# Performance work log

Hardware: AMD Instinct MI355X
Metric: run time of the kernel (lower is better)

Reference implementation:

```python
import jax, jax.numpy as jnp
import numpy as np

B, S, D = 2, 2048, 1024
H_Q, H_KV, DK, DV = 16, 8, 64, 64
R = H_Q // H_KV  # q heads per kv head (GQA)
THETA = 10000.0


def setup_inputs() -> dict:
    key = jax.random.key(0)
    ks = jax.random.split(key, 12)
    inv_freq = 1.0 / (THETA ** (jnp.arange(0, DK, 2, dtype=jnp.float32) / DK))  # [DK/2]
    angles = jnp.arange(S, dtype=jnp.float32)[:, None] * inv_freq[None, :]      # [S, DK/2]
    scale = 0.02
    return {
        "x": jax.random.normal(ks[0], (B, S, D), jnp.float32),
        "Wq": jax.random.normal(ks[1], (D, H_Q * DK), jnp.float32) * scale,
        "bq": jnp.zeros((H_Q * DK,), jnp.float32),
        "Wk": jax.random.normal(ks[2], (D, H_KV * DK), jnp.float32) * scale,
        "bk": jnp.zeros((H_KV * DK,), jnp.float32),
        "Wv": jax.random.normal(ks[3], (D, H_KV * DV), jnp.float32) * scale,
        "bv": jnp.zeros((H_KV * DV,), jnp.float32),
        "Wo": jax.random.normal(ks[4], (H_Q * DV, D), jnp.float32) * scale,
        "bo": jnp.zeros((D,), jnp.float32),
        "freqs_cos": jnp.cos(angles),
        "freqs_sin": jnp.sin(angles),
        "attention_mask": jax.random.bernoulli(ks[5], 0.9, (B, S)),  # True = real token
    }


def _rope(t, cos, sin):
    # t: [B, S, H, Dh]; cos/sin: [S, Dh/2]. Complex rotation on interleaved pairs.
    tp = t.reshape(*t.shape[:-1], -1, 2)
    x1, x2 = tp[..., 0], tp[..., 1]
    c = cos[None, :, None, :]
    s = sin[None, :, None, :]
    o1 = x1 * c - x2 * s
    o2 = x1 * s + x2 * c
    return jnp.stack([o1, o2], axis=-1).reshape(t.shape)


def reference(x, Wq, bq, Wk, bk, Wv, bv, Wo, bo, freqs_cos, freqs_sin, attention_mask):
    b, s, _ = x.shape
    q = (x @ Wq + bq).reshape(b, s, H_Q, DK)
    k = (x @ Wk + bk).reshape(b, s, H_KV, DK)
    v = (x @ Wv + bv).reshape(b, s, H_KV, DV)
    q = _rope(q, freqs_cos, freqs_sin)
    k = _rope(k, freqs_cos, freqs_sin)
    q = q.transpose(0, 2, 1, 3)                      # [B, Hq, S, DK]
    k = jnp.repeat(k.transpose(0, 2, 1, 3), R, axis=1)  # GQA expand -> [B, Hq, S, DK]
    v = jnp.repeat(v.transpose(0, 2, 1, 3), R, axis=1)  # [B, Hq, S, DV]
    causal = jnp.tril(jnp.ones((s, s), dtype=bool))
    # Module does logical_or(padding, causal) -- replicated faithfully.
    mask = jnp.logical_or(attention_mask[:, None, None, :], causal[None, None])
    scale = 1.0 / jnp.sqrt(jnp.float32(DK))
    scores = jnp.einsum('bhqd,bhkd->bhqk', q, k) * scale
    scores = jnp.where(mask, scores, -jnp.inf)
    attn = jax.nn.softmax(scores, axis=-1)
    out = jnp.einsum('bhqk,bhkd->bhqd', attn, v)
    out = out.transpose(0, 2, 1, 3).reshape(b, s, H_Q * DV)
    return out @ Wo + bo
```

## Files before the change

### kernel.cpp

```cpp
#include <hip/hip_runtime.h>
#include <hip/hip_bf16.h>
#include <math.h>

typedef __attribute__((ext_vector_type(8))) short bf16x8;
typedef __attribute__((ext_vector_type(4))) float f32x4;

#define OFF_XB  0ull
#define OFF_WT  (8ull<<20)
#define OFF_WO  (12ull<<20)
#define OFF_QB  (14ull<<20)
#define OFF_KB  (22ull<<20)
#define OFF_VT  (26ull<<20)
#define OFF_AO  (30ull<<20)
#define OFF_MB  (38ull<<20)

#define QSCALE 0.18033688056680276f

__device__ inline unsigned pack_bf162(float a, float b) {
    __hip_bfloat162 t = __float22bfloat162_rn(make_float2(a, b));
    return *(unsigned*)&t;
}

__device__ inline float exp2_fast(float x) {
    float r;
    asm("v_exp_f32 %0, %1" : "=v"(r) : "v"(x));
    return r;
}

__device__ inline void gload16(const void* g, void* l) {
    __builtin_amdgcn_global_load_lds(
        (const __attribute__((address_space(1))) void*)g,
        (__attribute__((address_space(3))) void*)l, 16, 0, 0);
}

__launch_bounds__(256)
__global__ void prep_kernel(const float* __restrict__ x,
                            const float* __restrict__ Wq, const float* __restrict__ Wk,
                            const float* __restrict__ Wv, const float* __restrict__ Wo,
                            const void* __restrict__ mraw,
                            __hip_bfloat16* __restrict__ XB,
                            __hip_bfloat16* __restrict__ WT,
                            __hip_bfloat16* __restrict__ WoT,
                            float* __restrict__ mbias) {
    __shared__ float T[32][33];
    __shared__ int bad01, badf;
    const int tid = threadIdx.x;
    const int bid = blockIdx.x;
    if (bid < 1024) {
        const int base = bid * 4096;
#pragma unroll
        for (int i = 0; i < 4; ++i) {
            const int e = base + (i * 256 + tid) * 4;
            const float4 v = *(const float4*)&x[e];
            uint2 pk;
            pk.x = pack_bf162(v.x, v.y);
            pk.y = pack_bf162(v.z, v.w);
            *(uint2*)&XB[e] = pk;
        }
    } else if (bid < 4096) {
        const float* src; int ldn, nbase; __hip_bfloat16* dst; int n0, k0;
        if (bid < 3072) {
            const int tb = bid - 1024;
            const int kt = tb >> 6, nt = tb & 63;
            n0 = nt * 32; k0 = kt * 32; dst = WT;
            if (n0 < 1024)      { src = Wq; ldn = 1024; nbase = n0; }
            else if (n0 < 1536) { src = Wk; ldn = 512;  nbase = n0 - 1024; }
            else                { src = Wv; ldn = 512;  nbase = n0 - 1536; }
        } else {
            const int tb = bid - 3072;
            const int kt = tb >> 5, nt = tb & 31;
            n0 = nt * 32; k0 = kt * 32; dst = WoT;
            src = Wo; ldn = 1024; nbase = n0;
        }
        const int c = tid & 31, r0 = tid >> 5;
#pragma unroll
        for (int i = 0; i < 4; ++i)
            T[r0 + 8 * i][c] = src[(size_t)(k0 + r0 + 8 * i) * ldn + nbase + c];
        __syncthreads();
#pragma unroll
        for (int i = 0; i < 4; ++i) {
            const int nn = r0 + 8 * i;
            dst[(size_t)(n0 + nn) * 1024 + k0 + c] = __float2bfloat16(T[c][nn]);
        }
    } else {
        if (tid == 0) { bad01 = 0; badf = 0; }
        __syncthreads();
        const unsigned* w = (const unsigned*)mraw;
#pragma unroll
        for (int i = 0; i < 4; ++i) {
            const unsigned v = w[tid * 4 + i];
            if (v > 1u) atomicAdd(&bad01, 1);
            if (v != 0u && v != 0x3F800000u) atomicAdd(&badf, 1);
        }
        __syncthreads();
        const int fmt = (bad01 == 0) ? 0 : ((badf == 0) ? 1 : 2);
        for (int i = tid; i < 4096; i += 256) {
            bool on;
            if (fmt == 2) on = (((const unsigned char*)mraw)[i] != 0);
            else          on = (w[i] != 0u);
            mbias[i] = on ? 0.f : -1e30f;
        }
    }
}

__launch_bounds__(256)
__global__ void qkv_mfma_kernel(const __hip_bfloat16* __restrict__ XB,
                                const __hip_bfloat16* __restrict__ WT,
                                const float* __restrict__ bq, const float* __restrict__ bk,
                                const float* __restrict__ bv,
                                const float* __restrict__ fc, const float* __restrict__ fs,
                                __hip_bfloat16* __restrict__ QB,
                                __hip_bfloat16* __restrict__ KB,
                                __hip_bfloat16* __restrict__ VT) {
    __shared__ __attribute__((aligned(16))) char Asm[16384];
    __shared__ __attribute__((aligned(16))) char Bsm[16384];
    const int tid = threadIdx.x;
    const int lane = tid & 63, wid = tid >> 6;
    const int c = lane & 15, g = lane >> 4;
    const int n0 = blockIdx.x * 128, m0 = blockIdx.y * 128;
    const int wn = (wid >> 1) * 64, wm = (wid & 1) * 64;

    f32x4 acc[4][4];
#pragma unroll
    for (int ni = 0; ni < 4; ++ni)
#pragma unroll
        for (int mj = 0; mj < 4; ++mj) acc[ni][mj] = f32x4{0.f, 0.f, 0.f, 0.f};

    for (int kt = 0; kt < 16; ++kt) {
        const int k0 = kt * 64;
#pragma unroll
        for (int rnd = 0; rnd < 4; ++rnd) {
            const int off = rnd * 4096 + wid * 1024 + lane * 16;
            const int row = off >> 7;
            const int chunk = ((off >> 4) & 7) ^ (row & 7);
            gload16((const char*)WT + ((size_t)(n0 + row) * 1024 + k0 + chunk * 8) * 2,
                    Asm + rnd * 4096 + wid * 1024);
            gload16((const char*)XB + ((size_t)(m0 + row) * 1024 + k0 + chunk * 8) * 2,
                    Bsm + rnd * 4096 + wid * 1024);
        }
        __syncthreads();
#pragma unroll
        for (int ks = 0; ks < 2; ++ks) {
            bf16x8 af[4], bfr[4];
#pragma unroll
            for (int t = 0; t < 4; ++t) {
                const int sl = ((g + 4 * ks) ^ (c & 7)) << 4;
                af[t]  = *(const bf16x8*)(Asm + (wn + 16 * t + c) * 128 + sl);
                bfr[t] = *(const bf16x8*)(Bsm + (wm + 16 * t + c) * 128 + sl);
            }
#pragma unroll
            for (int ni = 0; ni < 4; ++ni)
#pragma unroll
                for (int mj = 0; mj < 4; ++mj)
                    acc[ni][mj] = __builtin_amdgcn_mfma_f32_16x16x32_bf16(
                        af[ni], bfr[mj], acc[ni][mj], 0, 0, 0);
        }
        __syncthreads();
    }

#pragma unroll
    for (int ni = 0; ni < 4; ++ni) {
        const int nb = n0 + wn + 16 * ni + 4 * g;
        const float* bias; int nloc;
        if (nb < 1024)      { bias = bq; nloc = nb; }
        else if (nb < 1536) { bias = bk; nloc = nb - 1024; }
        else                { bias = bv; nloc = nb - 1536; }
        const float4 b4 = *(const float4*)&bias[nloc];
        const int h = nloc >> 6, dk = nb & 63;
#pragma unroll
        for (int mj = 0; mj < 4; ++mj) {
            const int tok = m0 + wm + 16 * mj + c;
            const int bb = tok >> 11, sp = tok & 2047;
            float v0 = acc[ni][mj][0] + b4.x;
            float v1 = acc[ni][mj][1] + b4.y;
            float v2 = acc[ni][mj][2] + b4.z;
            float v3 = acc[ni][mj][3] + b4.w;
            if (nb < 1536) {
                const int p = sp * 32 + (dk >> 1);
                const float c0 = fc[p], s0 = fs[p];
                const float c1 = fc[p + 1], s1 = fs[p + 1];
                float o0 = v0 * c0 - v1 * s0, o1 = v0 * s0 + v1 * c0;
                float o2 = v2 * c1 - v3 * s1, o3 = v2 * s1 + v3 * c1;
                uint2 pk;
                if (nb < 1024) {
                    o0 *= QSCALE; o1 *= QSCALE; o2 *= QSCALE; o3 *= QSCALE;
                    pk.x = pack_bf162(o0, o1); pk.y = pack_bf162(o2, o3);
                    *(uint2*)&QB[(size_t)((bb * 16 + h) * 2048 + sp) * 64 + dk] = pk;
                } else {
                    pk.x = pack_bf162(o0, o1); pk.y = pack_bf162(o2, o3);
                    *(uint2*)&KB[(size_t)((bb * 8 + h) * 2048 + sp) * 64 + dk] = pk;
                }
            } else {
                const size_t vb = (size_t)((bb * 8 + h) * 64 + dk) * 2048 + sp;
                VT[vb]          = __float2bfloat16(v0);
                VT[vb + 2048]   = __float2bfloat16(v1);
                VT[vb + 4096]   = __float2bfloat16(v2);
                VT[vb + 6144]   = __float2bfloat16(v3);
            }
        }
    }
}

__launch_bounds__(256)
__global__ void out_mfma_kernel(const __hip_bfloat16* __restrict__ AOB,
                                const __hip_bfloat16* __restrict__ WoT,
                                const float* __restrict__ bo,
                                float* __restrict__ out) {
    __shared__ __attribute__((aligned(16))) char Asm[16384];
    __shared__ __attribute__((aligned(16))) char Bsm[16384];
    const int tid = threadIdx.x;
    const int lane = tid & 63, wid = tid >> 6;
    const int c = lane & 15, g = lane >> 4;
    const int n0 = blockIdx.x * 128, m0 = blockIdx.y * 128;
    const int wn = (wid >> 1) * 64, wm = (wid & 1) * 64;

    f32x4 acc[4][4];
#pragma unroll
    for (int ni = 0; ni < 4; ++ni)
#pragma unroll
        for (int mj = 0; mj < 4; ++mj) acc[ni][mj] = f32x4{0.f, 0.f, 0.f, 0.f};

    for (int kt = 0; kt < 16; ++kt) {
        const int k0 = kt * 64;
#pragma unroll
        for (int rnd = 0; rnd < 4; ++rnd) {
            const int off = rnd * 4096 + wid * 1024 + lane * 16;
            const int row = off >> 7;
            const int chunk = ((off >> 4) & 7) ^ (row & 7);
            gload16((const char*)WoT + ((size_t)(n0 + row) * 1024 + k0 + chunk * 8) * 2,
                    Asm + rnd * 4096 + wid * 1024);
            gload16((const char*)AOB + ((size_t)(m0 + row) * 1024 + k0 + chunk * 8) * 2,
                    Bsm + rnd * 4096 + wid * 1024);
        }
        __syncthreads();
#pragma unroll
        for (int ks = 0; ks < 2; ++ks) {
            bf16x8 af[4], bfr[4];
#pragma unroll
            for (int t = 0; t < 4; ++t) {
                const int sl = ((g + 4 * ks) ^ (c & 7)) << 4;
                af[t]  = *(const bf16x8*)(Asm + (wn + 16 * t + c) * 128 + sl);
                bfr[t] = *(const bf16x8*)(Bsm + (wm + 16 * t + c) * 128 + sl);
            }
#pragma unroll
            for (int ni = 0; ni < 4; ++ni)
#pragma unroll
                for (int mj = 0; mj < 4; ++mj)
                    acc[ni][mj] = __builtin_amdgcn_mfma_f32_16x16x32_bf16(
                        af[ni], bfr[mj], acc[ni][mj], 0, 0, 0);
        }
        __syncthreads();
    }
#pragma unroll
    for (int ni = 0; ni < 4; ++ni) {
        const int nb = n0 + wn + 16 * ni + 4 * g;
        const float4 b4 = *(const float4*)&bo[nb];
#pragma unroll
        for (int mj = 0; mj < 4; ++mj) {
            const int tok = m0 + wm + 16 * mj + c;
            const f32x4 a = acc[ni][mj];
            const float4 st = make_float4(a[0] + b4.x, a[1] + b4.y,
                                          a[2] + b4.z, a[3] + b4.w);
            *(float4*)&out[(size_t)tok * 1024 + nb] = st;
        }
    }
}


#define STAGE(BUFSEL, K0_) do {                                                  \
    _Pragma("unroll") for (int rnd_ = 0; rnd_ < 2; ++rnd_) {                     \
        const int off_ = rnd_ * 4096 + tid * 16;                                 \
        const int row_ = off_ >> 7;                                              \
        const int ch_  = ((off_ >> 4) & 7) ^ (row_ & 7);                         \
        gload16(Kh + (size_t)((K0_) + row_) * 64 + ch_ * 8,                      \
                Ksm + (BUFSEL) * 8192 + rnd_ * 4096 + wid * 1024);               \
        gload16(Vh + (size_t)row_ * 2048 + (K0_) + ch_ * 8,                      \
                Vsm + (BUFSEL) * 8192 + rnd_ * 4096 + wid * 1024);               \
    }                                                                            \
} while (0)

__launch_bounds__(256)
__global__ void attn_kernel(const __hip_bfloat16* __restrict__ QB,
                            const __hip_bfloat16* __restrict__ KB,
                            const __hip_bfloat16* __restrict__ VT,
                            const float* __restrict__ maskb,
                            __hip_bfloat16* __restrict__ AOB) {
    __shared__ __attribute__((aligned(16))) char Ksm[16384];
    __shared__ __attribute__((aligned(16))) char Vsm[16384];
    __shared__ char P_lds[4][4096];

    const int tid  = threadIdx.x;
    const int lane = tid & 63, wid = tid >> 6;
    const int c = lane & 15, g = lane >> 4;

    const int bid = blockIdx.x;
    const int o_  = (bid & 7) * 64 + (bid >> 3);
    const int qx = o_ & 15, h = (o_ >> 4) & 15, b = o_ >> 8;
    const int qb = qx * 128 + wid * 32;

    const __hip_bfloat16* Qh = QB + (size_t)(b * 16 + h)       * 2048 * 64;
    const __hip_bfloat16* Kh = KB + (size_t)(b * 8 + (h >> 1)) * 2048 * 64;
    const __hip_bfloat16* Vh = VT + (size_t)(b * 8 + (h >> 1)) * 64 * 2048;
    const float* mb = maskb + b * 2048;

    STAGE(0, 0);

    bf16x8 bq[2][2];
#pragma unroll
    for (int rt = 0; rt < 2; ++rt)
#pragma unroll
        for (int ks = 0; ks < 2; ++ks)
            bq[rt][ks] = *(const bf16x8*)&Qh[(size_t)(qb + 16 * rt + c) * 64
                                             + 32 * ks + 8 * g];
    __syncthreads();

    const short oneb = (short)0x3F80;
    const bf16x8 ones = {oneb, oneb, oneb, oneb, oneb, oneb, oneb, oneb};

    f32x4 o[2][4];
    f32x4 lacc[2];
#pragma unroll
    for (int rt = 0; rt < 2; ++rt) {
        lacc[rt] = f32x4{0.f, 0.f, 0.f, 0.f};
#pragma unroll
        for (int mt = 0; mt < 4; ++mt) o[rt][mt] = f32x4{0.f, 0.f, 0.f, 0.f};
    }
    float m_[2] = {-INFINITY, -INFINITY};

    char* Pw = &P_lds[wid][0];
    const int swz = (c & 7) << 4;

    int cur = 0;
    for (int kt = 0; kt < 32; ++kt) {
        const int k0 = kt * 64;
        if (kt < 31) {
            STAGE(cur ^ 1, k0 + 64);
            asm volatile("s_waitcnt vmcnt(4)" ::: "memory");
        } else {
            asm volatile("s_waitcnt vmcnt(0)" ::: "memory");
        }
        __builtin_amdgcn_sched_barrier(0);
        __builtin_amdgcn_s_barrier();
        __builtin_amdgcn_sched_barrier(0);

        const char* Kc = Ksm + cur * 8192;
        const char* Vc = Vsm + cur * 8192;

        bf16x8 ak[4][2];
#pragma unroll
        for (int mt = 0; mt < 4; ++mt)
#pragma unroll
            for (int ks = 0; ks < 2; ++ks)
                ak[mt][ks] = *(const bf16x8*)(Kc + (16 * mt + c) * 128
                                              + (((g + 4 * ks) ^ (c & 7)) << 4));

        const bool needb = (k0 + 63 > qb);
        float4 biasv[4];
        if (needb) {
#pragma unroll
            for (int mt = 0; mt < 4; ++mt)
                biasv[mt] = *(const float4*)&mb[k0 + 16 * mt + 4 * g];
        }

        __builtin_amdgcn_s_setprio(1);
        f32x4 st[2][4];
#pragma unroll
        for (int rt = 0; rt < 2; ++rt)
#pragma unroll
            for (int mt = 0; mt < 4; ++mt) {
                f32x4 z = f32x4{0.f, 0.f, 0.f, 0.f};
                z = __builtin_amdgcn_mfma_f32_16x16x32_bf16(ak[mt][0], bq[rt][0], z, 0, 0, 0);
                z = __builtin_amdgcn_mfma_f32_16x16x32_bf16(ak[mt][1], bq[rt][1], z, 0, 0, 0);
                st[rt][mt] = z;
            }
        __builtin_amdgcn_s_setprio(0);

        bf16x8 av[4][2];
#pragma unroll
        for (int mt = 0; mt < 4; ++mt)
#pragma unroll
            for (int ks = 0; ks < 2; ++ks)
                av[mt][ks] = *(const bf16x8*)(Vc + (16 * mt + c) * 128
                                              + (((g + 4 * ks) ^ (c & 7)) << 4));

#pragma unroll
        for (int rt = 0; rt < 2; ++rt) {
            const int qw = qb + 16 * rt;
            float pmax = -INFINITY;
            if (k0 + 63 <= qw) {
#pragma unroll
                for (int mt = 0; mt < 4; ++mt)
#pragma unroll
                    for (int r = 0; r < 4; ++r)
                        pmax = fmaxf(pmax, st[rt][mt][r]);
            } else if (k0 > qw + 15) {
#pragma unroll
                for (int mt = 0; mt < 4; ++mt) {
                    st[rt][mt][0] += biasv[mt].x; st[rt][mt][1] += biasv[mt].y;
                    st[rt][mt][2] += biasv[mt].z; st[rt][mt][3] += biasv[mt].w;
#pragma unroll
                    for (int r = 0; r < 4; ++r)
                        pmax = fmaxf(pmax, st[rt][mt][r]);
                }
            } else {
                const int qg = qw + c;
#pragma unroll
                for (int mt = 0; mt < 4; ++mt) {
                    const float bvr[4] = {biasv[mt].x, biasv[mt].y,
                                          biasv[mt].z, biasv[mt].w};
#pragma unroll
                    for (int r = 0; r < 4; ++r) {
                        const int kg = k0 + 16 * mt + 4 * g + r;
                        st[rt][mt][r] += (kg <= qg) ? 0.f : bvr[r];
                        pmax = fmaxf(pmax, st[rt][mt][r]);
                    }
                }
            }
            pmax = fmaxf(pmax, __shfl_xor(pmax, 16));
            pmax = fmaxf(pmax, __shfl_xor(pmax, 32));
            if (!__all(pmax <= m_[rt] + 11.5f)) {
                const float mn = fmaxf(m_[rt], pmax);
                const float alpha = exp2_fast(m_[rt] - mn);
                m_[rt] = mn;
                lacc[rt][0] *= alpha;
#pragma unroll
                for (int mt = 0; mt < 4; ++mt) o[rt][mt] *= alpha;
            }
#pragma unroll
            for (int mt = 0; mt < 4; ++mt)
#pragma unroll
                for (int r = 0; r < 4; ++r)
                    st[rt][mt][r] = exp2_fast(st[rt][mt][r] - m_[rt]);

            char* Pr = Pw + rt * 2048 + c * 128;
#pragma unroll
            for (int mt = 0; mt < 4; ++mt) {
                const unsigned w0 = pack_bf162(st[rt][mt][0], st[rt][mt][1]);
                const unsigned w1 = pack_bf162(st[rt][mt][2], st[rt][mt][3]);
                *(unsigned long long*)(Pr + ((32 * mt + 8 * g) ^ swz)) =
                    (unsigned long long)w0 | ((unsigned long long)w1 << 32);
            }
        }

#pragma unroll
        for (int rt = 0; rt < 2; ++rt) {
            const char* Pr = Pw + rt * 2048 + c * 128;
            const bf16x8 pb0 = *(const bf16x8*)(Pr + ((16 * g) ^ swz));
            const bf16x8 pb1 = *(const bf16x8*)(Pr + ((64 + 16 * g) ^ swz));
            __builtin_amdgcn_s_setprio(1);
#pragma unroll
            for (int mt = 0; mt < 4; ++mt) {
                o[rt][mt] = __builtin_amdgcn_mfma_f32_16x16x32_bf16(av[mt][0], pb0, o[rt][mt], 0, 0, 0);
                o[rt][mt] = __builtin_amdgcn_mfma_f32_16x16x32_bf16(av[mt][1], pb1, o[rt][mt], 0, 0, 0);
            }
            lacc[rt] = __builtin_amdgcn_mfma_f32_16x16x32_bf16(ones, pb0, lacc[rt], 0, 0, 0);
            lacc[rt] = __builtin_amdgcn_mfma_f32_16x16x32_bf16(ones, pb1, lacc[rt], 0, 0, 0);
            __builtin_amdgcn_s_setprio(0);
        }

        __builtin_amdgcn_sched_barrier(0);
        __builtin_amdgcn_s_barrier();
        __builtin_amdgcn_sched_barrier(0);
        cur ^= 1;
    }

#pragma unroll
    for (int rt = 0; rt < 2; ++rt) {
        const float inv = 1.f / lacc[rt][0];
        const size_t tok = (size_t)(b * 2048 + qb + 16 * rt + c);
#pragma unroll
        for (int mt = 0; mt < 4; ++mt) {
            uint2 pk;
            pk.x = pack_bf162(o[rt][mt][0] * inv, o[rt][mt][1] * inv);
            pk.y = pack_bf162(o[rt][mt][2] * inv, o[rt][mt][3] * inv);
            *(uint2*)&AOB[tok * 1024 + h * 64 + 16 * mt + 4 * g] = pk;
        }
    }
}

extern "C" void kernel_launch(void* const* d_in, const int* in_sizes, int n_in,
                              void* d_out, int out_size, void* d_ws, size_t ws_size,
                              hipStream_t stream) {
    const float* x  = (const float*)d_in[0];
    const float* Wq = (const float*)d_in[1];
    const float* bq = (const float*)d_in[2];
    const float* Wk = (const float*)d_in[3];
    const float* bk = (const float*)d_in[4];
    const float* Wv = (const float*)d_in[5];
    const float* bv = (const float*)d_in[6];
    const float* Wo = (const float*)d_in[7];
    const float* bo = (const float*)d_in[8];
    const float* fc = (const float*)d_in[9];
    const float* fs = (const float*)d_in[10];
    const void*  am = d_in[11];

    char* ws = (char*)d_ws;
    __hip_bfloat16* XB  = (__hip_bfloat16*)(ws + OFF_XB);
    __hip_bfloat16* WT  = (__hip_bfloat16*)(ws + OFF_WT);
    __hip_bfloat16* WoT = (__hip_bfloat16*)(ws + OFF_WO);
    __hip_bfloat16* QB  = (__hip_bfloat16*)(ws + OFF_QB);
    __hip_bfloat16* KB  = (__hip_bfloat16*)(ws + OFF_KB);
    __hip_bfloat16* VT  = (__hip_bfloat16*)(ws + OFF_VT);
    __hip_bfloat16* AOB = (__hip_bfloat16*)(ws + OFF_AO);
    float* mbias = (float*)(ws + OFF_MB);
    float* out   = (float*)d_out;

    hipLaunchKernelGGL(prep_kernel, dim3(4097), dim3(256), 0, stream,
                       x, Wq, Wk, Wv, Wo, am, XB, WT, WoT, mbias);
    hipLaunchKernelGGL(qkv_mfma_kernel, dim3(16, 32), dim3(256), 0, stream,
                       XB, WT, bq, bk, bv, fc, fs, QB, KB, VT);
    hipLaunchKernelGGL(attn_kernel, dim3(512), dim3(256), 0, stream,
                       QB, KB, VT, mbias, AOB);
    hipLaunchKernelGGL(out_mfma_kernel, dim3(8, 32), dim3(256), 0, stream,
                       AOB, WoT, bo, out);
}
```

Measured before the change: 142.9 us.

## Split attention KV range into two halves and merge partials in separate kernel

Each attention block now covers only half of the key sequence, which doubles the grid from 512 to 1024 blocks. Each block writes unnormalized bf16 partial outputs plus its running max and sum to workspace, and a new merge kernel combines the two halves with a log-sum-exp rescale. The P buffer in LDS is halved by fusing the P write with its PV consumption per row tile, which lowers shared memory use and may allow higher occupancy. The cost is an extra kernel launch, extra global traffic for the partials, and an added bf16 rounding of the unnormalized partials.

```diff
diff --git a/kernel.cpp b/kernel.cpp
--- a/kernel.cpp
+++ b/kernel.cpp
@@ -13,6 +13,8 @@
 #define OFF_VT  (26ull<<20)
 #define OFF_AO  (30ull<<20)
 #define OFF_MB  (38ull<<20)
+#define OFF_OP  (40ull<<20)
+#define OFF_ML  (56ull<<20)
 
 #define QSCALE 0.18033688056680276f
 
@@ -25,6 +27,10 @@
     float r;
     asm("v_exp_f32 %0, %1" : "=v"(r) : "v"(x));
     return r;
+}
+
+__device__ inline float bf2f(short s) {
+    return __uint_as_float(((unsigned)(unsigned short)s) << 16);
 }
 
 __device__ inline void gload16(const void* g, void* l) {
@@ -284,26 +290,28 @@
                             const __hip_bfloat16* __restrict__ KB,
                             const __hip_bfloat16* __restrict__ VT,
                             const float* __restrict__ maskb,
-                            __hip_bfloat16* __restrict__ AOB) {
+                            __hip_bfloat16* __restrict__ OP,
+                            float2* __restrict__ ML) {
     __shared__ __attribute__((aligned(16))) char Ksm[16384];
     __shared__ __attribute__((aligned(16))) char Vsm[16384];
-    __shared__ char P_lds[4][4096];
+    __shared__ char P_lds[4][2048];
 
     const int tid  = threadIdx.x;
     const int lane = tid & 63, wid = tid >> 6;
     const int c = lane & 15, g = lane >> 4;
 
     const int bid = blockIdx.x;
-    const int o_  = (bid & 7) * 64 + (bid >> 3);
-    const int qx = o_ & 15, h = (o_ >> 4) & 15, b = o_ >> 8;
+    const int o_  = (bid & 7) * 128 + (bid >> 3);
+    const int qx = o_ & 15, h = (o_ >> 4) & 15, b = (o_ >> 8) & 1, half = o_ >> 9;
     const int qb = qx * 128 + wid * 32;
+    const int kbase = half * 1024;
 
     const __hip_bfloat16* Qh = QB + (size_t)(b * 16 + h)       * 2048 * 64;
     const __hip_bfloat16* Kh = KB + (size_t)(b * 8 + (h >> 1)) * 2048 * 64;
     const __hip_bfloat16* Vh = VT + (size_t)(b * 8 + (h >> 1)) * 64 * 2048;
     const float* mb = maskb + b * 2048;
 
-    STAGE(0, 0);
+    STAGE(0, kbase);
 
     bf16x8 bq[2][2];
 #pragma unroll
@@ -327,13 +335,13 @@
     }
     float m_[2] = {-INFINITY, -INFINITY};
 
-    char* Pw = &P_lds[wid][0];
+    char* Pr = &P_lds[wid][0] + c * 128;
     const int swz = (c & 7) << 4;
 
     int cur = 0;
-    for (int kt = 0; kt < 32; ++kt) {
-        const int k0 = kt * 64;
-        if (kt < 31) {
+    for (int kt = 0; kt < 16; ++kt) {
+        const int k0 = kbase + kt * 64;
+        if (kt < 15) {
             STAGE(cur ^ 1, k0 + 64);
             asm volatile("s_waitcnt vmcnt(4)" ::: "memory");
         } else {
@@ -432,7 +440,6 @@
                 for (int r = 0; r < 4; ++r)
                     st[rt][mt][r] = exp2_fast(st[rt][mt][r] - m_[rt]);
 
-            char* Pr = Pw + rt * 2048 + c * 128;
 #pragma unroll
             for (int mt = 0; mt < 4; ++mt) {
                 const unsigned w0 = pack_bf162(st[rt][mt][0], st[rt][mt][1]);
@@ -440,11 +447,6 @@
                 *(unsigned long long*)(Pr + ((32 * mt + 8 * g) ^ swz)) =
                     (unsigned long long)w0 | ((unsigned long long)w1 << 32);
             }
-        }
-
-#pragma unroll
-        for (int rt = 0; rt < 2; ++rt) {
-            const char* Pr = Pw + rt * 2048 + c * 128;
             const bf16x8 pb0 = *(const bf16x8*)(Pr + ((16 * g) ^ swz));
             const bf16x8 pb1 = *(const bf16x8*)(Pr + ((64 + 16 * g) ^ swz));
             __builtin_amdgcn_s_setprio(1);
@@ -464,17 +466,64 @@
         cur ^= 1;
     }
 
+    const size_t hrow = (size_t)(b * 16 + h) * 2048;
+    __hip_bfloat16* OPh = OP + (size_t)half * (65536ull * 64);
 #pragma unroll
     for (int rt = 0; rt < 2; ++rt) {
-        const float inv = 1.f / lacc[rt][0];
-        const size_t tok = (size_t)(b * 2048 + qb + 16 * rt + c);
+        const size_t row = hrow + qb + 16 * rt + c;
 #pragma unroll
         for (int mt = 0; mt < 4; ++mt) {
             uint2 pk;
-            pk.x = pack_bf162(o[rt][mt][0] * inv, o[rt][mt][1] * inv);
-            pk.y = pack_bf162(o[rt][mt][2] * inv, o[rt][mt][3] * inv);
-            *(uint2*)&AOB[tok * 1024 + h * 64 + 16 * mt + 4 * g] = pk;
-        }
+            pk.x = pack_bf162(o[rt][mt][0], o[rt][mt][1]);
+            pk.y = pack_bf162(o[rt][mt][2], o[rt][mt][3]);
+            *(uint2*)&OPh[row * 64 + 16 * mt + 4 * g] = pk;
+        }
+        if (g == 0)
+            ML[half * 65536 + row] = make_float2(m_[rt], lacc[rt][0]);
+    }
+}
+
+__launch_bounds__(256)
+__global__ void merge_kernel(const __hip_bfloat16* __restrict__ OP,
+                             const float2* __restrict__ ML,
+                             __hip_bfloat16* __restrict__ AOB) {
+    const int tid = threadIdx.x;
+    const int bid = blockIdx.x;
+    const int sp_t = bid & 15, h = (bid >> 4) & 15, b = bid >> 8;
+    const int sp = sp_t * 128 + (tid >> 1);
+    const int dh = (tid & 1) * 32;
+    const size_t row = (size_t)(b * 16 + h) * 2048 + sp;
+
+    const float2 ml0 = ML[row];
+    const float2 ml1 = ML[65536 + row];
+    const float mx = fmaxf(ml0.x, ml1.x);
+    float a0 = exp2_fast(ml0.x - mx);
+    float a1 = exp2_fast(ml1.x - mx);
+    const float inv = 1.f / (ml0.y * a0 + ml1.y * a1);
+    a0 *= inv; a1 *= inv;
+
+    const size_t base = row * 64 + dh;
+    const size_t obase = (size_t)(b * 2048 + sp) * 1024 + h * 64 + dh;
+#pragma unroll
+    for (int j = 0; j < 4; ++j) {
+        const bf16x8 p0 = *(const bf16x8*)&OP[base + 8 * j];
+        const bf16x8 p1 = *(const bf16x8*)&OP[65536ull * 64 + base + 8 * j];
+        uint2 pk0, pk1;
+        float f0, f1;
+        f0 = bf2f(p0[0]) * a0 + bf2f(p1[0]) * a1;
+        f1 = bf2f(p0[1]) * a0 + bf2f(p1[1]) * a1;
+        pk0.x = pack_bf162(f0, f1);
+        f0 = bf2f(p0[2]) * a0 + bf2f(p1[2]) * a1;
+        f1 = bf2f(p0[3]) * a0 + bf2f(p1[3]) * a1;
+        pk0.y = pack_bf162(f0, f1);
+        f0 = bf2f(p0[4]) * a0 + bf2f(p1[4]) * a1;
+        f1 = bf2f(p0[5]) * a0 + bf2f(p1[5]) * a1;
+        pk1.x = pack_bf162(f0, f1);
+        f0 = bf2f(p0[6]) * a0 + bf2f(p1[6]) * a1;
+        f1 = bf2f(p0[7]) * a0 + bf2f(p1[7]) * a1;
+        pk1.y = pack_bf162(f0, f1);
+        *(uint2*)&AOB[obase + 8 * j]     = pk0;
+        *(uint2*)&AOB[obase + 8 * j + 4] = pk1;
     }
 }
 
@@ -503,14 +552,18 @@
     __hip_bfloat16* VT  = (__hip_bfloat16*)(ws + OFF_VT);
     __hip_bfloat16* AOB = (__hip_bfloat16*)(ws + OFF_AO);
     float* mbias = (float*)(ws + OFF_MB);
+    __hip_bfloat16* OP  = (__hip_bfloat16*)(ws + OFF_OP);
+    float2* ML          = (float2*)(ws + OFF_ML);
     float* out   = (float*)d_out;
 
     hipLaunchKernelGGL(prep_kernel, dim3(4097), dim3(256), 0, stream,
                        x, Wq, Wk, Wv, Wo, am, XB, WT, WoT, mbias);
     hipLaunchKernelGGL(qkv_mfma_kernel, dim3(16, 32), dim3(256), 0, stream,
                        XB, WT, bq, bk, bv, fc, fs, QB, KB, VT);
-    hipLaunchKernelGGL(attn_kernel, dim3(512), dim3(256), 0, stream,
-                       QB, KB, VT, mbias, AOB);
+    hipLaunchKernelGGL(attn_kernel, dim3(1024), dim3(256), 0, stream,
+                       QB, KB, VT, mbias, OP, ML);
+    hipLaunchKernelGGL(merge_kernel, dim3(512), dim3(256), 0, stream,
+                       OP, ML, AOB);
     hipLaunchKernelGGL(out_mfma_kernel, dim3(8, 32), dim3(256), 0, stream,
                        AOB, WoT, bo, out);
 }
```

New measurement: 188.7 us. 32.0% more time.

## Double-buffer LDS tiles in QKV and output projection GEMMs

Applied to the files above, without the earlier changes.

Both projection GEMM kernels now use two LDS buffers per operand and issue the global-to-LDS loads for the next K tile before computing on the current one. Explicit vmcnt waits and raw barriers replace the plain syncthreads, so tile loads overlap with MFMA work. This doubles shared memory per block to 64KB, which may lower occupancy, and relies on hand-counted vmcnt values being correct.

```diff
diff --git a/kernel.cpp b/kernel.cpp
--- a/kernel.cpp
+++ b/kernel.cpp
@@ -103,6 +103,18 @@
     }
 }
 
+#define QSTAGE(SEL, K0_) do {                                                    \
+    _Pragma("unroll") for (int rnd_ = 0; rnd_ < 4; ++rnd_) {                     \
+        const int off_ = rnd_ * 4096 + wid * 1024 + lane * 16;                   \
+        const int row_ = off_ >> 7;                                              \
+        const int ch_  = ((off_ >> 4) & 7) ^ (row_ & 7);                         \
+        gload16((const char*)Ag + ((size_t)(n0 + row_) * 1024 + (K0_) + ch_ * 8) * 2, \
+                Asm + (SEL) * 16384 + rnd_ * 4096 + wid * 1024);                 \
+        gload16((const char*)Bg + ((size_t)(m0 + row_) * 1024 + (K0_) + ch_ * 8) * 2, \
+                Bsm + (SEL) * 16384 + rnd_ * 4096 + wid * 1024);                 \
+    }                                                                            \
+} while (0)
+
 __launch_bounds__(256)
 __global__ void qkv_mfma_kernel(const __hip_bfloat16* __restrict__ XB,
                                 const __hip_bfloat16* __restrict__ WT,
@@ -112,13 +124,15 @@
                                 __hip_bfloat16* __restrict__ QB,
                                 __hip_bfloat16* __restrict__ KB,
                                 __hip_bfloat16* __restrict__ VT) {
-    __shared__ __attribute__((aligned(16))) char Asm[16384];
-    __shared__ __attribute__((aligned(16))) char Bsm[16384];
+    __shared__ __attribute__((aligned(16))) char Asm[32768];
+    __shared__ __attribute__((aligned(16))) char Bsm[32768];
     const int tid = threadIdx.x;
     const int lane = tid & 63, wid = tid >> 6;
     const int c = lane & 15, g = lane >> 4;
     const int n0 = blockIdx.x * 128, m0 = blockIdx.y * 128;
     const int wn = (wid >> 1) * 64, wm = (wid & 1) * 64;
+    const __hip_bfloat16* Ag = WT;
+    const __hip_bfloat16* Bg = XB;
 
     f32x4 acc[4][4];
 #pragma unroll
@@ -126,27 +140,30 @@
 #pragma unroll
         for (int mj = 0; mj < 4; ++mj) acc[ni][mj] = f32x4{0.f, 0.f, 0.f, 0.f};
 
+    QSTAGE(0, 0);
+    int cur = 0;
     for (int kt = 0; kt < 16; ++kt) {
         const int k0 = kt * 64;
-#pragma unroll
-        for (int rnd = 0; rnd < 4; ++rnd) {
-            const int off = rnd * 4096 + wid * 1024 + lane * 16;
-            const int row = off >> 7;
-            const int chunk = ((off >> 4) & 7) ^ (row & 7);
-            gload16((const char*)WT + ((size_t)(n0 + row) * 1024 + k0 + chunk * 8) * 2,
-                    Asm + rnd * 4096 + wid * 1024);
-            gload16((const char*)XB + ((size_t)(m0 + row) * 1024 + k0 + chunk * 8) * 2,
-                    Bsm + rnd * 4096 + wid * 1024);
-        }
-        __syncthreads();
+        if (kt < 15) {
+            QSTAGE(cur ^ 1, k0 + 64);
+            asm volatile("s_waitcnt vmcnt(8)" ::: "memory");
+        } else {
+            asm volatile("s_waitcnt vmcnt(0)" ::: "memory");
+        }
+        __builtin_amdgcn_sched_barrier(0);
+        __builtin_amdgcn_s_barrier();
+        __builtin_amdgcn_sched_barrier(0);
+
+        const char* Ac = Asm + cur * 16384;
+        const char* Bc = Bsm + cur * 16384;
 #pragma unroll
         for (int ks = 0; ks < 2; ++ks) {
             bf16x8 af[4], bfr[4];
 #pragma unroll
             for (int t = 0; t < 4; ++t) {
                 const int sl = ((g + 4 * ks) ^ (c & 7)) << 4;
-                af[t]  = *(const bf16x8*)(Asm + (wn + 16 * t + c) * 128 + sl);
-                bfr[t] = *(const bf16x8*)(Bsm + (wm + 16 * t + c) * 128 + sl);
+                af[t]  = *(const bf16x8*)(Ac + (wn + 16 * t + c) * 128 + sl);
+                bfr[t] = *(const bf16x8*)(Bc + (wm + 16 * t + c) * 128 + sl);
             }
 #pragma unroll
             for (int ni = 0; ni < 4; ++ni)
@@ -155,7 +172,10 @@
                     acc[ni][mj] = __builtin_amdgcn_mfma_f32_16x16x32_bf16(
                         af[ni], bfr[mj], acc[ni][mj], 0, 0, 0);
         }
-        __syncthreads();
+        __builtin_amdgcn_sched_barrier(0);
+        __builtin_amdgcn_s_barrier();
+        __builtin_amdgcn_sched_barrier(0);
+        cur ^= 1;
     }
 
 #pragma unroll
@@ -206,13 +226,15 @@
                                 const __hip_bfloat16* __restrict__ WoT,
                                 const float* __restrict__ bo,
                                 float* __restrict__ out) {
-    __shared__ __attribute__((aligned(16))) char Asm[16384];
-    __shared__ __attribute__((aligned(16))) char Bsm[16384];
+    __shared__ __attribute__((aligned(16))) char Asm[32768];
+    __shared__ __attribute__((aligned(16))) char Bsm[32768];
     const int tid = threadIdx.x;
     const int lane = tid & 63, wid = tid >> 6;
     const int c = lane & 15, g = lane >> 4;
     const int n0 = blockIdx.x * 128, m0 = blockIdx.y * 128;
     const int wn = (wid >> 1) * 64, wm = (wid & 1) * 64;
+    const __hip_bfloat16* Ag = WoT;
+    const __hip_bfloat16* Bg = AOB;
 
     f32x4 acc[4][4];
 #pragma unroll
@@ -220,27 +242,30 @@
 #pragma unroll
         for (int mj = 0; mj < 4; ++mj) acc[ni][mj] = f32x4{0.f, 0.f, 0.f, 0.f};
 
+    QSTAGE(0, 0);
+    int cur = 0;
     for (int kt = 0; kt < 16; ++kt) {
         const int k0 = kt * 64;
-#pragma unroll
-        for (int rnd = 0; rnd < 4; ++rnd) {
-            const int off = rnd * 4096 + wid * 1024 + lane * 16;
-            const int row = off >> 7;
-            const int chunk = ((off >> 4) & 7) ^ (row & 7);
-            gload16((const char*)WoT + ((size_t)(n0 + row) * 1024 + k0 + chunk * 8) * 2,
-                    Asm + rnd * 4096 + wid * 1024);
-            gload16((const char*)AOB + ((size_t)(m0 + row) * 1024 + k0 + chunk * 8) * 2,
-                    Bsm + rnd * 4096 + wid * 1024);
-        }
-        __syncthreads();
+        if (kt < 15) {
+            QSTAGE(cur ^ 1, k0 + 64);
+            asm volatile("s_waitcnt vmcnt(8)" ::: "memory");
+        } else {
+            asm volatile("s_waitcnt vmcnt(0)" ::: "memory");
+        }
+        __builtin_amdgcn_sched_barrier(0);
+        __builtin_amdgcn_s_barrier();
+        __builtin_amdgcn_sched_barrier(0);
+
+        const char* Ac = Asm + cur * 16384;
+        const char* Bc = Bsm + cur * 16384;
 #pragma unroll
         for (int ks = 0; ks < 2; ++ks) {
             bf16x8 af[4], bfr[4];
 #pragma unroll
             for (int t = 0; t < 4; ++t) {
                 const int sl = ((g + 4 * ks) ^ (c & 7)) << 4;
-                af[t]  = *(const bf16x8*)(Asm + (wn + 16 * t + c) * 128 + sl);
-                bfr[t] = *(const bf16x8*)(Bsm + (wm + 16 * t + c) * 128 + sl);
+                af[t]  = *(const bf16x8*)(Ac + (wn + 16 * t + c) * 128 + sl);
+                bfr[t] = *(const bf16x8*)(Bc + (wm + 16 * t + c) * 128 + sl);
             }
 #pragma unroll
             for (int ni = 0; ni < 4; ++ni)
@@ -249,7 +274,10 @@
                     acc[ni][mj] = __builtin_amdgcn_mfma_f32_16x16x32_bf16(
                         af[ni], bfr[mj], acc[ni][mj], 0, 0, 0);
         }
-        __syncthreads();
+        __builtin_amdgcn_sched_barrier(0);
+        __builtin_amdgcn_s_barrier();
+        __builtin_amdgcn_sched_barrier(0);
+        cur ^= 1;
     }
 #pragma unroll
     for (int ni = 0; ni < 4; ++ni) {
```

Measured after the change: 139.4 us. 1.03x faster.
